# Kernel tuning notes

Measured on AMD Instinct MI355X. Metric: run time of the kernel, lower is better.

Reference implementation:

```python
import jax, jax.numpy as jnp
import numpy as np

EPS = 1e-6  # F.cosine_similarity eps


def setup_inputs() -> dict:
    key = jax.random.key(0)
    kx, = jax.random.split(key, 1)
    N, M, D = 1024, 32, 256
    x = jax.random.normal(kx, (N, M, D), dtype=jnp.float32)
    w = jnp.array([10.0], dtype=jnp.float32)  # init_w
    b = jnp.array([-5.0], dtype=jnp.float32)  # init_b
    return {"x": x, "w": w, "b": b}


def _ge2e_softmax_loss(x, w, b):
    N, M, D = x.shape
    # centroids over all utterances of each speaker: (N, D)
    cent = x.mean(axis=1)
    # modified centroid excluding utterance i (used when k == j): (N, M, D)
    mod_cent = (x.sum(axis=1, keepdims=True) - x) / (M - 1)

    x_norm = jnp.linalg.norm(x, axis=-1)          # (N, M)
    cent_norm = jnp.linalg.norm(cent, axis=-1)    # (N,)
    mod_norm = jnp.linalg.norm(mod_cent, axis=-1) # (N, M)

    # off-diagonal cosine sim via one batched matmul: (N, M, N)
    dots = jnp.einsum('nmd,kd->nmk', x, cent)
    sim = dots / jnp.maximum(x_norm[:, :, None] * cent_norm[None, None, :], EPS)

    # diagonal (k == j) uses the modified centroid: (N, M)
    diag_sim = jnp.sum(x * mod_cent, axis=-1) / jnp.maximum(x_norm * mod_norm, EPS)

    # splice modified-centroid sims onto the k == j diagonal
    eye = jnp.eye(N, dtype=bool)[:, None, :]  # (N, 1, N)
    S = jnp.where(eye, diag_sim[:, :, None], sim)  # (N, M, N)

    calc = w[0] * S + b[0]
    # L = -S_{ji,j} + logsumexp_k S_{ji,k}
    diag_calc = w[0] * diag_sim + b[0]
    loss = (-diag_calc + jax.nn.logsumexp(calc, axis=-1)).sum()
    return loss


def reference(x, w, b):
    return _ge2e_softmax_loss(x, w, b)
```

## Files before the change

kernel.cpp:

```cpp
#include <hip/hip_runtime.h>
#include <hip/hip_bf16.h>
#include <math.h>

typedef float f32x4 __attribute__((ext_vector_type(4)));
typedef short short8 __attribute__((ext_vector_type(8)));

#define GEPS 1e-6f

static __device__ __forceinline__ short8 ldb8(const unsigned short* p) {
  return *reinterpret_cast<const short8*>(p);
}

static __device__ __forceinline__ void bfsplit(float v, unsigned short& h, unsigned short& l) {
  __hip_bfloat16 hb = __float2bfloat16(v);
  h = *reinterpret_cast<unsigned short*>(&hb);
  float r = v - __bfloat162float(hb);
  __hip_bfloat16 lb = __float2bfloat16(r);
  l = *reinterpret_cast<unsigned short*>(&lb);
}

__global__ __launch_bounds__(256) void k1_prep(
    const float* __restrict__ x,
    unsigned short* __restrict__ xhg, unsigned short* __restrict__ xlg,
    unsigned short* __restrict__ chg, unsigned short* __restrict__ clg,
    float* __restrict__ invcn, float* __restrict__ xn, float* __restrict__ dsim)
{
  const int n = blockIdx.x;
  const int tid = threadIdx.x;
  const int c4 = tid & 63;
  const int mq = tid >> 6;
  __shared__ f32x4 part[4][64];

  f32x4 xr[8];
  f32x4 ps = (f32x4){0.f, 0.f, 0.f, 0.f};
  const size_t nbase = (size_t)n * 8192;

  #pragma unroll
  for (int p = 0; p < 8; ++p) {
    const int m = mq * 8 + p;
    const size_t off = nbase + m * 256 + c4 * 4;
    f32x4 v = *reinterpret_cast<const f32x4*>(x + off);
    xr[p] = v;
    ps += v;
    ushort4 hv, lv;
    bfsplit(v.x, hv.x, lv.x);
    bfsplit(v.y, hv.y, lv.y);
    bfsplit(v.z, hv.z, lv.z);
    bfsplit(v.w, hv.w, lv.w);
    *reinterpret_cast<ushort4*>(xhg + off) = hv;
    *reinterpret_cast<ushort4*>(xlg + off) = lv;
  }
  part[mq][c4] = ps;
  __syncthreads();

  f32x4 sl = part[0][c4] + part[1][c4] + part[2][c4] + part[3][c4];

  if (mq == 0) {
    f32x4 c = sl * 0.03125f;
    ushort4 hv, lv;
    bfsplit(c.x, hv.x, lv.x);
    bfsplit(c.y, hv.y, lv.y);
    bfsplit(c.z, hv.z, lv.z);
    bfsplit(c.w, hv.w, lv.w);
    *reinterpret_cast<ushort4*>(chg + n * 256 + c4 * 4) = hv;
    *reinterpret_cast<ushort4*>(clg + n * 256 + c4 * 4) = lv;
  }

  float s2 = sl.x * sl.x + sl.y * sl.y + sl.z * sl.z + sl.w * sl.w;
  #pragma unroll
  for (int off = 32; off; off >>= 1) s2 += __shfl_xor(s2, off, 64);
  if (tid == 0) invcn[n] = 32.0f / sqrtf(s2);

  #pragma unroll
  for (int p = 0; p < 8; ++p) {
    const f32x4 v = xr[p];
    float a1 = v.x * v.x + v.y * v.y + v.z * v.z + v.w * v.w;
    float sx = v.x * sl.x + v.y * sl.y + v.z * sl.z + v.w * sl.w;
    #pragma unroll
    for (int off = 32; off; off >>= 1) {
      a1 += __shfl_xor(a1, off, 64);
      sx += __shfl_xor(sx, off, 64);
    }
    if (c4 == 0) {
      const int m = mq * 8 + p;
      const float a2 = (sx - a1) * (1.0f / 31.0f);
      const float a3 = (s2 - 2.0f * sx + a1) * (1.0f / 961.0f);
      const float xnv = sqrtf(a1);
      const float mn  = sqrtf(a3);
      xn[n * 32 + m]   = xnv;
      dsim[n * 32 + m] = a2 / fmaxf(xnv * mn, GEPS);
    }
  }
}

__global__ __launch_bounds__(256, 3) void k2_mfma(
    const unsigned short* __restrict__ xhg, const unsigned short* __restrict__ xlg,
    const unsigned short* __restrict__ chg, const unsigned short* __restrict__ clg,
    const float* __restrict__ invcn, const float* __restrict__ xn,
    const float* __restrict__ dsim, const float* __restrict__ wp,
    const float* __restrict__ bp, float* __restrict__ row_sum)
{
  const int bid = blockIdx.x;
  const int rowbase = (bid >> 2) * 64;
  const int cq = bid & 3;
  const int tid = threadIdx.x;
  const int wv = tid >> 6;
  const int lane = tid & 63;
  const int q = lane >> 4;
  const int l15 = lane & 15;
  const int colbase = cq * 256 + wv * 64;

  __shared__ float rs[64];
  if (tid < 64) rs[tid] = 0.f;
  __syncthreads();

  f32x4 acc[4][4];
  #pragma unroll
  for (int mt = 0; mt < 4; ++mt)
    #pragma unroll
    for (int kt = 0; kt < 4; ++kt) acc[mt][kt] = (f32x4){0.f, 0.f, 0.f, 0.f};

  #pragma unroll 1
  for (int ck = 0; ck < 8; ++ck) {
    const int d0 = ck * 32 + q * 8;
    short8 a_h[4], a_l[4], b_h[4], b_l[4];
    #pragma unroll
    for (int mt = 0; mt < 4; ++mt) {
      const size_t abase = (size_t)(rowbase + mt * 16 + l15) * 256 + d0;
      a_h[mt] = ldb8(xhg + abase);
      a_l[mt] = ldb8(xlg + abase);
    }
    #pragma unroll
    for (int kt = 0; kt < 4; ++kt) {
      const size_t bbase = (size_t)(colbase + kt * 16 + l15) * 256 + d0;
      b_h[kt] = ldb8(chg + bbase);
      b_l[kt] = ldb8(clg + bbase);
    }
    #pragma unroll
    for (int mt = 0; mt < 4; ++mt)
      #pragma unroll
      for (int kt = 0; kt < 4; ++kt)
        acc[mt][kt] = __builtin_amdgcn_mfma_f32_16x16x32_bf16(a_l[mt], b_h[kt], acc[mt][kt], 0, 0, 0);
    #pragma unroll
    for (int mt = 0; mt < 4; ++mt)
      #pragma unroll
      for (int kt = 0; kt < 4; ++kt)
        acc[mt][kt] = __builtin_amdgcn_mfma_f32_16x16x32_bf16(a_h[mt], b_l[kt], acc[mt][kt], 0, 0, 0);
    #pragma unroll
    for (int mt = 0; mt < 4; ++mt)
      #pragma unroll
      for (int kt = 0; kt < 4; ++kt)
        acc[mt][kt] = __builtin_amdgcn_mfma_f32_16x16x32_bf16(a_h[mt], b_h[kt], acc[mt][kt], 0, 0, 0);
  }

  const float w = wp[0], b = bp[0];
  const float B = fabsf(w) + fabsf(b);
  const float L2E = 1.44269504088896f;
  const float u = (b - B) * L2E;
  const float wl = w * L2E;

  #pragma unroll
  for (int mt = 0; mt < 4; ++mt) {
    const int nrow = (rowbase + mt * 16) >> 5;
    #pragma unroll
    for (int r = 0; r < 4; ++r) {
      const int grow = rowbase + mt * 16 + q * 4 + r;
      const float srow = wl / xn[grow];
      const float ediag = fmaf(dsim[grow], wl, u);
      float S = 0.f;
      #pragma unroll
      for (int kt = 0; kt < 4; ++kt) {
        const int colg = colbase + kt * 16 + l15;
        float p = exp2f(fmaf(acc[mt][kt][r] * srow, invcn[colg], u));
        if (colg == nrow) p = exp2f(ediag);
        S += p;
      }
      S += __shfl_xor(S, 1, 64);
      S += __shfl_xor(S, 2, 64);
      S += __shfl_xor(S, 4, 64);
      S += __shfl_xor(S, 8, 64);
      if (l15 == 0) atomicAdd(&rs[mt * 16 + q * 4 + r], S);
    }
  }
  __syncthreads();
  if (tid < 64) atomicAdd(&row_sum[rowbase + tid], rs[tid]);
}

__global__ __launch_bounds__(256) void k3_final(
    const float* __restrict__ dsim, const float* __restrict__ row_sum,
    const float* __restrict__ wp, const float* __restrict__ bp,
    float* __restrict__ out)
{
  const int r = blockIdx.x * 256 + threadIdx.x;
  const float w = wp[0], b = bp[0];
  const float B = fabsf(w) + fabsf(b);
  float v = -fmaf(w, dsim[r], b) + B + logf(row_sum[r]);
  #pragma unroll
  for (int off = 32; off; off >>= 1) v += __shfl_xor(v, off, 64);
  __shared__ float red[4];
  const int lane = threadIdx.x & 63, wv = threadIdx.x >> 6;
  if (lane == 0) red[wv] = v;
  __syncthreads();
  if (threadIdx.x == 0) atomicAdd(out, red[0] + red[1] + red[2] + red[3]);
}

extern "C" void kernel_launch(void* const* d_in, const int* in_sizes, int n_in,
                              void* d_out, int out_size, void* d_ws, size_t ws_size,
                              hipStream_t stream)
{
  const float* x = (const float*)d_in[0];
  const float* w = (const float*)d_in[1];
  const float* b = (const float*)d_in[2];
  float* out = (float*)d_out;

  char* W = (char*)d_ws;
  unsigned short* xhg = (unsigned short*)(W);
  unsigned short* xlg = (unsigned short*)(W + 16777216);
  unsigned short* chg = (unsigned short*)(W + 33554432);
  unsigned short* clg = (unsigned short*)(W + 34078720);
  float* invcn  = (float*)(W + 34603008);
  float* xn     = (float*)(W + 34607104);
  float* dsim   = (float*)(W + 34738176);
  float* rowsum = (float*)(W + 34869248);

  hipMemsetAsync(rowsum, 0, 32768 * sizeof(float), stream);
  hipMemsetAsync(out, 0, sizeof(float), stream);
  k1_prep<<<1024, 256, 0, stream>>>(x, xhg, xlg, chg, clg, invcn, xn, dsim);
  k2_mfma<<<2048, 256, 0, stream>>>(xhg, xlg, chg, clg, invcn, xn, dsim, w, b, rowsum);
  k3_final<<<128, 256, 0, stream>>>(dsim, rowsum, w, b, out);
}
```

Measured before the change: 223.8 us.

## Double-buffer MFMA operand loads, XCD-aware block swizzle, and wider prep stores

The k2 main loop now uses two register buffer sets so the global loads for the next K chunk are issued before the MFMAs on the current chunk, hiding load latency. Launch bounds drop from 3 to 2 blocks per SM to leave registers for the second buffer set. Block IDs are remapped so the four column-quarter blocks sharing a row group land on the same XCD, improving L2 reuse of the row tiles. k1 switches to 8-element-per-thread loads and stores with a 32-lane reduction, which means fewer, wider memory transactions. The trade-off is higher register pressure and lower occupancy in k2.

```diff
diff --git a/kernel.cpp b/kernel.cpp
--- a/kernel.cpp
+++ b/kernel.cpp
@@ -4,6 +4,7 @@
 
 typedef float f32x4 __attribute__((ext_vector_type(4)));
 typedef short short8 __attribute__((ext_vector_type(8)));
+typedef unsigned short ushort8v __attribute__((ext_vector_type(8)));
 
 #define GEPS 1e-6f
 
@@ -27,62 +28,81 @@
 {
   const int n = blockIdx.x;
   const int tid = threadIdx.x;
-  const int c4 = tid & 63;
-  const int mq = tid >> 6;
-  __shared__ f32x4 part[4][64];
-
-  f32x4 xr[8];
-  f32x4 ps = (f32x4){0.f, 0.f, 0.f, 0.f};
+  const int dg = tid & 31;
+  const int mrow = tid >> 5;
+  __shared__ f32x4 part[2][8][32];
+
   const size_t nbase = (size_t)n * 8192;
-
-  #pragma unroll
-  for (int p = 0; p < 8; ++p) {
-    const int m = mq * 8 + p;
-    const size_t off = nbase + m * 256 + c4 * 4;
-    f32x4 v = *reinterpret_cast<const f32x4*>(x + off);
-    xr[p] = v;
-    ps += v;
-    ushort4 hv, lv;
-    bfsplit(v.x, hv.x, lv.x);
-    bfsplit(v.y, hv.y, lv.y);
-    bfsplit(v.z, hv.z, lv.z);
-    bfsplit(v.w, hv.w, lv.w);
-    *reinterpret_cast<ushort4*>(xhg + off) = hv;
-    *reinterpret_cast<ushort4*>(xlg + off) = lv;
-  }
-  part[mq][c4] = ps;
-  __syncthreads();
-
-  f32x4 sl = part[0][c4] + part[1][c4] + part[2][c4] + part[3][c4];
-
-  if (mq == 0) {
-    f32x4 c = sl * 0.03125f;
-    ushort4 hv, lv;
-    bfsplit(c.x, hv.x, lv.x);
-    bfsplit(c.y, hv.y, lv.y);
-    bfsplit(c.z, hv.z, lv.z);
-    bfsplit(c.w, hv.w, lv.w);
-    *reinterpret_cast<ushort4*>(chg + n * 256 + c4 * 4) = hv;
-    *reinterpret_cast<ushort4*>(clg + n * 256 + c4 * 4) = lv;
-  }
-
-  float s2 = sl.x * sl.x + sl.y * sl.y + sl.z * sl.z + sl.w * sl.w;
-  #pragma unroll
-  for (int off = 32; off; off >>= 1) s2 += __shfl_xor(s2, off, 64);
+  f32x4 xa0[4], xa1[4];
+  f32x4 ps0 = (f32x4){0.f,0.f,0.f,0.f}, ps1 = (f32x4){0.f,0.f,0.f,0.f};
+
+  #pragma unroll
+  for (int mi = 0; mi < 4; ++mi) {
+    const int m = mi * 8 + mrow;
+    const size_t off = nbase + m * 256 + dg * 8;
+    f32x4 v0 = *reinterpret_cast<const f32x4*>(x + off);
+    f32x4 v1 = *reinterpret_cast<const f32x4*>(x + off + 4);
+    xa0[mi] = v0; xa1[mi] = v1;
+    ps0 += v0; ps1 += v1;
+    ushort8v hv, lv;
+    #pragma unroll
+    for (int e = 0; e < 4; ++e) {
+      unsigned short h, l;
+      bfsplit(v0[e], h, l); hv[e] = h; lv[e] = l;
+    }
+    #pragma unroll
+    for (int e = 0; e < 4; ++e) {
+      unsigned short h, l;
+      bfsplit(v1[e], h, l); hv[4+e] = h; lv[4+e] = l;
+    }
+    *reinterpret_cast<ushort8v*>(xhg + off) = hv;
+    *reinterpret_cast<ushort8v*>(xlg + off) = lv;
+  }
+  part[0][mrow][dg] = ps0;
+  part[1][mrow][dg] = ps1;
+  __syncthreads();
+
+  f32x4 sl0 = (f32x4){0.f,0.f,0.f,0.f}, sl1 = (f32x4){0.f,0.f,0.f,0.f};
+  #pragma unroll
+  for (int mr = 0; mr < 8; ++mr) { sl0 += part[0][mr][dg]; sl1 += part[1][mr][dg]; }
+
+  if (tid < 32) {
+    f32x4 c0 = sl0 * 0.03125f, c1 = sl1 * 0.03125f;
+    ushort8v hv, lv;
+    #pragma unroll
+    for (int e = 0; e < 4; ++e) {
+      unsigned short h, l;
+      bfsplit(c0[e], h, l); hv[e] = h; lv[e] = l;
+    }
+    #pragma unroll
+    for (int e = 0; e < 4; ++e) {
+      unsigned short h, l;
+      bfsplit(c1[e], h, l); hv[4+e] = h; lv[4+e] = l;
+    }
+    *reinterpret_cast<ushort8v*>(chg + n * 256 + dg * 8) = hv;
+    *reinterpret_cast<ushort8v*>(clg + n * 256 + dg * 8) = lv;
+  }
+
+  float s2 = sl0.x*sl0.x + sl0.y*sl0.y + sl0.z*sl0.z + sl0.w*sl0.w
+           + sl1.x*sl1.x + sl1.y*sl1.y + sl1.z*sl1.z + sl1.w*sl1.w;
+  #pragma unroll
+  for (int off = 16; off; off >>= 1) s2 += __shfl_xor(s2, off, 64);
   if (tid == 0) invcn[n] = 32.0f / sqrtf(s2);
 
   #pragma unroll
-  for (int p = 0; p < 8; ++p) {
-    const f32x4 v = xr[p];
-    float a1 = v.x * v.x + v.y * v.y + v.z * v.z + v.w * v.w;
-    float sx = v.x * sl.x + v.y * sl.y + v.z * sl.z + v.w * sl.w;
-    #pragma unroll
-    for (int off = 32; off; off >>= 1) {
+  for (int mi = 0; mi < 4; ++mi) {
+    const f32x4 v0 = xa0[mi], v1 = xa1[mi];
+    float a1 = v0.x*v0.x + v0.y*v0.y + v0.z*v0.z + v0.w*v0.w
+             + v1.x*v1.x + v1.y*v1.y + v1.z*v1.z + v1.w*v1.w;
+    float sx = v0.x*sl0.x + v0.y*sl0.y + v0.z*sl0.z + v0.w*sl0.w
+             + v1.x*sl1.x + v1.y*sl1.y + v1.z*sl1.z + v1.w*sl1.w;
+    #pragma unroll
+    for (int off = 16; off; off >>= 1) {
       a1 += __shfl_xor(a1, off, 64);
       sx += __shfl_xor(sx, off, 64);
     }
-    if (c4 == 0) {
-      const int m = mq * 8 + p;
+    if (dg == 0) {
+      const int m = mi * 8 + mrow;
       const float a2 = (sx - a1) * (1.0f / 31.0f);
       const float a3 = (s2 - 2.0f * sx + a1) * (1.0f / 961.0f);
       const float xnv = sqrtf(a1);
@@ -93,7 +113,7 @@
   }
 }
 
-__global__ __launch_bounds__(256, 3) void k2_mfma(
+__global__ __launch_bounds__(256, 2) void k2_mfma(
     const unsigned short* __restrict__ xhg, const unsigned short* __restrict__ xlg,
     const unsigned short* __restrict__ chg, const unsigned short* __restrict__ clg,
     const float* __restrict__ invcn, const float* __restrict__ xn,
@@ -101,8 +121,11 @@
     const float* __restrict__ bp, float* __restrict__ row_sum)
 {
   const int bid = blockIdx.x;
-  const int rowbase = (bid >> 2) * 64;
-  const int cq = bid & 3;
+  const int xcd = bid & 7;
+  const int slot = bid >> 3;
+  const int rgrp = xcd + 8 * (slot >> 2);
+  const int cq = slot & 3;
+  const int rowbase = rgrp * 64;
   const int tid = threadIdx.x;
   const int wv = tid >> 6;
   const int lane = tid & 63;
@@ -114,43 +137,62 @@
   if (tid < 64) rs[tid] = 0.f;
   __syncthreads();
 
+  size_t abase[4], bbase[4];
+  #pragma unroll
+  for (int mt = 0; mt < 4; ++mt)
+    abase[mt] = (size_t)(rowbase + mt * 16 + l15) * 256 + q * 8;
+  #pragma unroll
+  for (int kt = 0; kt < 4; ++kt)
+    bbase[kt] = (size_t)(colbase + kt * 16 + l15) * 256 + q * 8;
+
   f32x4 acc[4][4];
   #pragma unroll
   for (int mt = 0; mt < 4; ++mt)
     #pragma unroll
-    for (int kt = 0; kt < 4; ++kt) acc[mt][kt] = (f32x4){0.f, 0.f, 0.f, 0.f};
-
+    for (int kt = 0; kt < 4; ++kt) acc[mt][kt] = (f32x4){0.f,0.f,0.f,0.f};
+
+  auto LOAD = [&](int ck, short8 (&ah)[4], short8 (&al)[4],
+                  short8 (&bh)[4], short8 (&bl)[4]) {
+    const int off = ck * 32;
+    #pragma unroll
+    for (int mt = 0; mt < 4; ++mt) {
+      ah[mt] = ldb8(xhg + abase[mt] + off);
+      al[mt] = ldb8(xlg + abase[mt] + off);
+    }
+    #pragma unroll
+    for (int kt = 0; kt < 4; ++kt) {
+      bh[kt] = ldb8(chg + bbase[kt] + off);
+      bl[kt] = ldb8(clg + bbase[kt] + off);
+    }
+  };
+  auto MFMA3 = [&](short8 (&ah)[4], short8 (&al)[4],
+                   short8 (&bh)[4], short8 (&bl)[4]) {
+    #pragma unroll
+    for (int mt = 0; mt < 4; ++mt)
+      #pragma unroll
+      for (int kt = 0; kt < 4; ++kt)
+        acc[mt][kt] = __builtin_amdgcn_mfma_f32_16x16x32_bf16(al[mt], bh[kt], acc[mt][kt], 0, 0, 0);
+    #pragma unroll
+    for (int mt = 0; mt < 4; ++mt)
+      #pragma unroll
+      for (int kt = 0; kt < 4; ++kt)
+        acc[mt][kt] = __builtin_amdgcn_mfma_f32_16x16x32_bf16(ah[mt], bl[kt], acc[mt][kt], 0, 0, 0);
+    #pragma unroll
+    for (int mt = 0; mt < 4; ++mt)
+      #pragma unroll
+      for (int kt = 0; kt < 4; ++kt)
+        acc[mt][kt] = __builtin_amdgcn_mfma_f32_16x16x32_bf16(ah[mt], bh[kt], acc[mt][kt], 0, 0, 0);
+  };
+
+  short8 ahA[4], alA[4], bhA[4], blA[4];
+  short8 ahB[4], alB[4], bhB[4], blB[4];
+  LOAD(0, ahA, alA, bhA, blA);
   #pragma unroll 1
-  for (int ck = 0; ck < 8; ++ck) {
-    const int d0 = ck * 32 + q * 8;
-    short8 a_h[4], a_l[4], b_h[4], b_l[4];
-    #pragma unroll
-    for (int mt = 0; mt < 4; ++mt) {
-      const size_t abase = (size_t)(rowbase + mt * 16 + l15) * 256 + d0;
-      a_h[mt] = ldb8(xhg + abase);
-      a_l[mt] = ldb8(xlg + abase);
-    }
-    #pragma unroll
-    for (int kt = 0; kt < 4; ++kt) {
-      const size_t bbase = (size_t)(colbase + kt * 16 + l15) * 256 + d0;
-      b_h[kt] = ldb8(chg + bbase);
-      b_l[kt] = ldb8(clg + bbase);
-    }
-    #pragma unroll
-    for (int mt = 0; mt < 4; ++mt)
-      #pragma unroll
-      for (int kt = 0; kt < 4; ++kt)
-        acc[mt][kt] = __builtin_amdgcn_mfma_f32_16x16x32_bf16(a_l[mt], b_h[kt], acc[mt][kt], 0, 0, 0);
-    #pragma unroll
-    for (int mt = 0; mt < 4; ++mt)
-      #pragma unroll
-      for (int kt = 0; kt < 4; ++kt)
-        acc[mt][kt] = __builtin_amdgcn_mfma_f32_16x16x32_bf16(a_h[mt], b_l[kt], acc[mt][kt], 0, 0, 0);
-    #pragma unroll
-    for (int mt = 0; mt < 4; ++mt)
-      #pragma unroll
-      for (int kt = 0; kt < 4; ++kt)
-        acc[mt][kt] = __builtin_amdgcn_mfma_f32_16x16x32_bf16(a_h[mt], b_h[kt], acc[mt][kt], 0, 0, 0);
+  for (int t = 0; t < 4; ++t) {
+    LOAD(2 * t + 1, ahB, alB, bhB, blB);
+    MFMA3(ahA, alA, bhA, blA);
+    if (t < 3) LOAD(2 * t + 2, ahA, alA, bhA, blA);
+    MFMA3(ahB, alB, bhB, blB);
   }
 
   const float w = wp[0], b = bp[0];
```

Measured after the change: 222.7 us. About the same (-0.5%).
